# Performance work log

Measured on AMD Instinct MI355X. Metric: run time of the kernel, lower is better.

The kernel has to match this reference:

```python
import jax, jax.numpy as jnp
import numpy as np

B, T, D = 4, 2048, 1024
H, DH = 16, 64

def setup_inputs() -> dict:
    key = jax.random.key(0)
    k1, k2, k3 = jax.random.split(key, 3)
    x = jax.random.normal(k1, (B, T, D), dtype=jnp.float32)
    ln_gamma = jnp.ones((D,), dtype=jnp.float32)
    ln_beta = jnp.zeros((D,), dtype=jnp.float32)
    W_qkv = jax.random.normal(k2, (3 * D, D), dtype=jnp.float32) * (1.0 / np.sqrt(D))
    W_o = jax.random.normal(k3, (D, D), dtype=jnp.float32) * (1.0 / np.sqrt(D))
    return {"x": x, "ln_gamma": ln_gamma, "ln_beta": ln_beta, "W_qkv": W_qkv, "W_o": W_o}

def reference(x, ln_gamma, ln_beta, W_qkv, W_o):
    b, t, d = x.shape
    scale = 1.0 / np.sqrt(DH)
    # pre-LN in fp32 (eps=1e-5, elementwise affine)
    xf = x.astype(jnp.float32)
    mu = jnp.mean(xf, axis=-1, keepdims=True)
    var = jnp.mean(jnp.square(xf - mu), axis=-1, keepdims=True)
    xn = (xf - mu) * jax.lax.rsqrt(var + 1e-5) * ln_gamma + ln_beta
    xn = xn.astype(x.dtype)
    # fused QKV projection (torch Linear: y = x @ W^T), view as (B,T,H,3*DH)
    qkv = jnp.einsum('btd,ed->bte', xn, W_qkv).reshape(b, t, H, 3 * DH)
    Q, K, V = jnp.split(qkv, 3, axis=-1)  # each (B,T,H,DH)
    # scores (B,H,T,T), causal mask, softmax
    scores = jnp.einsum('bqhd,bkhd->bhqk', Q, K) * scale
    causal = jnp.tril(jnp.ones((t, t), dtype=bool))
    scores = jnp.where(causal, scores, -jnp.inf)
    A = jax.nn.softmax(scores, axis=-1)
    ctx = jnp.einsum('bhqk,bkhd->bqhd', A, V).reshape(b, t, d)
    return jnp.einsum('btd,ed->bte', ctx, W_o)
```

## Files before the change

kernel.cpp:

```cpp
#include <hip/hip_runtime.h>


typedef __attribute__((ext_vector_type(8))) short bf8v;
typedef __attribute__((ext_vector_type(4))) float f4v;

#define Tt  2048
#define Dd  1024
#define Hh  16
#define DHh 64

#if __has_builtin(__builtin_amdgcn_exp2f)
#define EXP2(x) __builtin_amdgcn_exp2f(x)
#else
#define EXP2(x) __expf((x) * 0.69314718056f)
#endif

__device__ __forceinline__ ushort f2bf(float f) {
  union { float f; unsigned v; } c; c.f = f;
  unsigned r = c.v + 0x7fffu + ((c.v >> 16) & 1u);
  return (ushort)(r >> 16);
}
__device__ __forceinline__ ushort f2bf_rn(float f) {
  union { float f; unsigned v; } c; c.f = f;
  return (ushort)((c.v + 0x8000u) >> 16);
}
__device__ __forceinline__ f4v zero4() { f4v z; z[0]=z[1]=z[2]=z[3]=0.f; return z; }

__device__ __forceinline__ void gl_lds16(const ushort* g, ushort* l) {
  __builtin_amdgcn_global_load_lds(
      (const __attribute__((address_space(1))) unsigned*)g,
      (__attribute__((address_space(3))) unsigned*)l, 16, 0, 0);
}

__global__ __launch_bounds__(256)
void prep_k(const float* __restrict__ wqkv, ushort* __restrict__ wqkb,
            const float* __restrict__ wo,   ushort* __restrict__ wob,
            const float* __restrict__ x, const float* __restrict__ g,
            const float* __restrict__ bta, ushort* __restrict__ xn) {
  const int bid = blockIdx.x, tid = threadIdx.x;
  if (bid < 4096) {
    const float4* src = (bid < 3072) ? (const float4*)wqkv : (const float4*)wo;
    ushort4* dst      = (bid < 3072) ? (ushort4*)wqkb : (ushort4*)wob;
    const int i = ((bid < 3072) ? bid : (bid - 3072)) * 256 + tid;
    const float4 v = src[i];
    ushort4 o;
    o.x = f2bf(v.x); o.y = f2bf(v.y); o.z = f2bf(v.z); o.w = f2bf(v.w);
    dst[i] = o;
    return;
  }
  const int row = bid - 4096;
  const float4 v = ((const float4*)(x + row * Dd))[tid];
  float s  = v.x + v.y + v.z + v.w;
  float sq = v.x*v.x + v.y*v.y + v.z*v.z + v.w*v.w;
  #pragma unroll
  for (int off = 32; off; off >>= 1) {
    s  += __shfl_down(s,  off, 64);
    sq += __shfl_down(sq, off, 64);
  }
  __shared__ float red[8];
  const int w = tid >> 6, l = tid & 63;
  if (l == 0) { red[w] = s; red[w + 4] = sq; }
  __syncthreads();
  s  = red[0] + red[1] + red[2] + red[3];
  sq = red[4] + red[5] + red[6] + red[7];
  const float mu  = s * (1.0f / Dd);
  const float var = sq * (1.0f / Dd) - mu * mu;
  const float rs  = rsqrtf(var + 1e-5f);
  const float4 gv = ((const float4*)g)[tid];
  const float4 bv = ((const float4*)bta)[tid];
  ushort4 o;
  o.x = f2bf((v.x - mu) * rs * gv.x + bv.x);
  o.y = f2bf((v.y - mu) * rs * gv.y + bv.y);
  o.z = f2bf((v.z - mu) * rs * gv.z + bv.z);
  o.w = f2bf((v.w - mu) * rs * gv.w + bv.w);
  ((ushort4*)(xn + row * Dd))[tid] = o;
}

template<int MODE>
__global__ __launch_bounds__(256)
void gemm128(const ushort* __restrict__ A, const ushort* __restrict__ Bt,
             void* __restrict__ O0v, ushort* __restrict__ O1, ushort* __restrict__ O2,
             int Kd, int nbm) {
  __shared__ ushort As[2][128 * 64], Bs[2][128 * 64];
  const int tid = threadIdx.x;
  const int l = tid & 63, w = tid >> 6, fr = l & 15, fq = l >> 4;
  const int wm = w & 1, wn = w >> 1;
  const int bm = blockIdx.x % nbm, bn = blockIdx.x / nbm;
  const int gr8 = l >> 3, gc8s = ((l & 7) ^ gr8) * 8;
  const int sw = fr & 7;
  const int cA = (fq ^ sw) * 8, cB = ((4 + fq) ^ sw) * 8;
  const int NIT = Kd >> 6;

  f4v acc[4][4];
  #pragma unroll
  for (int m = 0; m < 4; m++)
    #pragma unroll
    for (int n = 0; n < 4; n++) acc[m][n] = zero4();

  auto stage = [&](int it, int bi) {
    const int k0 = it * 64;
    #pragma unroll
    for (int i = 0; i < 4; i++) {
      const int row = w * 32 + i * 8;
      gl_lds16(A  + (bm * 128 + row + gr8) * Kd + k0 + gc8s, &As[bi][row * 64]);
      gl_lds16(Bt + (bn * 128 + row + gr8) * Kd + k0 + gc8s, &Bs[bi][row * 64]);
    }
  };

  stage(0, 0);
  for (int it = 0; it < NIT; ++it) {
    __syncthreads();
    if (it + 1 < NIT) stage(it + 1, (it + 1) & 1);
    const ushort* Ab = As[it & 1];
    const ushort* Bb = Bs[it & 1];
    #pragma unroll
    for (int kk = 0; kk < 2; kk++) {
      const int cs = kk ? cB : cA;
      bf8v af[4], bf[4];
      #pragma unroll
      for (int m = 0; m < 4; m++)
        af[m] = *(const bf8v*)&Ab[(wm * 64 + m * 16 + fr) * 64 + cs];
      #pragma unroll
      for (int n = 0; n < 4; n++)
        bf[n] = *(const bf8v*)&Bb[(wn * 64 + n * 16 + fr) * 64 + cs];
      #pragma unroll
      for (int m = 0; m < 4; m++)
        #pragma unroll
        for (int n = 0; n < 4; n++)
          acc[m][n] = __builtin_amdgcn_mfma_f32_16x16x32_bf16(af[m], bf[n], acc[m][n], 0, 0, 0);
    }
  }

  #pragma unroll
  for (int m = 0; m < 4; m++) {
    const int grow = bm * 128 + wm * 64 + m * 16 + fq * 4;
    #pragma unroll
    for (int n = 0; n < 4; n++) {
      const int e = bn * 128 + wn * 64 + n * 16 + fr;
      #pragma unroll
      for (int r = 0; r < 4; r++) {
        const int row = grow + r;
        if (MODE == 0) {
          const int h = e / 192, inner = e % 192;
          const int sel = inner >> 6, dh = inner & 63;
          if (sel == 2) continue;
          const int bb = row >> 11, t = row & 2047;
          float v = acc[m][n][r];
          if (sel == 0) v *= 0.18033688f;
          ushort* dst = (sel == 0) ? (ushort*)O0v : O1;
          dst[((bb * Hh + h) * Tt + t) * DHh + dh] = f2bf(v);
        } else {
          ((float*)O0v)[row * Dd + e] = acc[m][n][r];
        }
      }
    }
  }

  if (MODE == 0) {
    const int bnm3 = bn % 3;
    if (bnm3 != 0) {
      const int vrun = (bnm3 == 1) ? 0 : 1;
      ushort* Vl = &As[0][0];
      __syncthreads();
      if (wn == vrun) {
        #pragma unroll
        for (int m = 0; m < 4; m++) {
          const int row0 = wm * 64 + m * 16 + fq * 4;
          #pragma unroll
          for (int n = 0; n < 4; n++) {
            const int col = n * 16 + fr;
            ushort4 pk;
            pk.x = f2bf(acc[m][n][0]); pk.y = f2bf(acc[m][n][1]);
            pk.z = f2bf(acc[m][n][2]); pk.w = f2bf(acc[m][n][3]);
            *(ushort4*)&Vl[col * 140 + row0] = pk;
          }
        }
      }
      __syncthreads();
      const int evr = bn * 128 + vrun * 64;
      const int hq  = evr / 192;
      const int bb  = bm >> 4, t0g = (bm & 15) * 128;
      ushort* vdst = O2 + (bb * Hh + hq) * (size_t)(DHh * Tt) + t0g;
      #pragma unroll
      for (int i = 0; i < 4; i++) {
        const int u = i * 256 + tid;
        const int dh = u >> 4, tc = (u & 15) * 8;
        const ushort4 lo = *(const ushort4*)&Vl[dh * 140 + tc];
        const ushort4 hi = *(const ushort4*)&Vl[dh * 140 + tc + 4];
        union { ushort s[8]; uint4 v; } pk;
        pk.s[0] = lo.x; pk.s[1] = lo.y; pk.s[2] = lo.z; pk.s[3] = lo.w;
        pk.s[4] = hi.x; pk.s[5] = hi.y; pk.s[6] = hi.z; pk.s[7] = hi.w;
        *(uint4*)&vdst[dh * Tt + tc] = pk.v;
      }
    }
  }
}

__global__ __launch_bounds__(512)
void attn_k(const ushort* __restrict__ Qb, const ushort* __restrict__ Kb,
            const ushort* __restrict__ Vtg, ushort* __restrict__ ctx) {
  __shared__ ushort QS[128 * 64];
  __shared__ ushort Pb[128 * 68];
  __shared__ ushort Ks[2][64 * 64], Vt[2][64 * 64];
  const int tid = threadIdx.x;
  const int l = tid & 63, w = tid >> 6, fr = l & 15, fq = l >> 4;
  const int bid = blockIdx.x;
  const int hb = (bid & 7) * 8 + (bid >> 6);
  const int u  = (bid >> 3) & 7;
  const int h  = hb & 15, b = hb >> 4;
  const int headbase = hb * Tt * DHh;
  const int gr8 = l >> 3, gc8s = ((l & 7) ^ gr8) * 8;
  const int sw = fr & 7;
  const int cA = (fq ^ sw) * 8, cB = ((4 + fq) ^ sw) * 8;

  auto stageKV = [&](int kt, int bi) {
    const int row = w * 8;
    gl_lds16(Kb  + headbase + (kt * 64 + row + gr8) * DHh + gc8s, &Ks[bi][row * 64]);
    gl_lds16(Vtg + headbase + (row + gr8) * Tt + kt * 64 + gc8s, &Vt[bi][row * 64]);
  };

  for (int half = 0; half < 2; ++half) {
    const int qt = half ? (15 - u) : u;
    const int qrow0w = qt * 128 + w * 16;

    if (half) __syncthreads();

    #pragma unroll
    for (int i = 0; i < 2; i++) {
      const int row = w * 16 + i * 8;
      gl_lds16(Qb + headbase + (qt * 128 + row + gr8) * DHh + gc8s, &QS[row * 64]);
    }
    stageKV(0, 0);
    __syncthreads();

    bf8v aq[2];
    aq[0] = *(const bf8v*)&QS[(w * 16 + fr) * 64 + cA];
    aq[1] = *(const bf8v*)&QS[(w * 16 + fr) * 64 + cB];
    __asm__ __volatile__("" ::: "memory");

    f4v o[4];
    #pragma unroll
    for (int n = 0; n < 4; n++) o[n] = zero4();
    float lsum = 0.f;

    const int ktmax = 2 * qt + 1;
    for (int kt = 0; kt <= ktmax; ++kt) {
      if (kt) __syncthreads();
      if (kt < ktmax) stageKV(kt + 1, (kt + 1) & 1);
      const ushort* K_ = Ks[kt & 1];
      const ushort* V_ = Vt[kt & 1];

      if (kt * 64 <= qrow0w + 15) {
        f4v scT[4];
        #pragma unroll
        for (int n = 0; n < 4; n++) scT[n] = zero4();
        __builtin_amdgcn_s_setprio(1);
        #pragma unroll
        for (int nt = 0; nt < 4; nt++) {
          const bf8v k0 = *(const bf8v*)&K_[(nt * 16 + fr) * 64 + cA];
          const bf8v k1 = *(const bf8v*)&K_[(nt * 16 + fr) * 64 + cB];
          scT[nt] = __builtin_amdgcn_mfma_f32_16x16x32_bf16(k0, aq[0], scT[nt], 0, 0, 0);
          scT[nt] = __builtin_amdgcn_mfma_f32_16x16x32_bf16(k1, aq[1], scT[nt], 0, 0, 0);
        }
        __builtin_amdgcn_s_setprio(0);

        if (kt * 64 + 63 > qrow0w) {
          const int q0 = qrow0w + fr;
          #pragma unroll
          for (int nt = 0; nt < 4; nt++) {
            const int kc0 = kt * 64 + nt * 16 + fq * 4;
            #pragma unroll
            for (int r = 0; r < 4; r++)
              if (kc0 + r > q0) scT[nt][r] = -1e30f;
          }
        }

        {
          const int prow = w * 16 + fr;
          ushort* pbase = &Pb[prow * 68 + fq * 4];
          #pragma unroll
          for (int nt = 0; nt < 4; nt++) {
            const float p0 = EXP2(scT[nt][0]), p1 = EXP2(scT[nt][1]);
            const float p2 = EXP2(scT[nt][2]), p3 = EXP2(scT[nt][3]);
            ushort4 pk;
            pk.x = f2bf_rn(p0); pk.y = f2bf_rn(p1);
            pk.z = f2bf_rn(p2); pk.w = f2bf_rn(p3);
            *(ushort4*)(pbase + nt * 16) = pk;
            lsum += (p0 + p1) + (p2 + p3);
          }
        }

        __asm__ __volatile__("" ::: "memory");

        __builtin_amdgcn_s_setprio(1);
        #pragma unroll
        for (int s = 0; s < 2; s++) {
          const bf8v ap = *(const bf8v*)&Pb[(w * 16 + fr) * 68 + s * 32 + fq * 8];
          #pragma unroll
          for (int nt = 0; nt < 4; nt++) {
            const bf8v bv2 = *(const bf8v*)&V_[(nt * 16 + fr) * 64 + (s ? cB : cA)];
            o[nt] = __builtin_amdgcn_mfma_f32_16x16x32_bf16(ap, bv2, o[nt], 0, 0, 0);
          }
        }
        __builtin_amdgcn_s_setprio(0);
      }
    }

    float t = lsum;
    t += __shfl_xor(t, 16, 64);
    t += __shfl_xor(t, 32, 64);
    const float inv = 1.0f / t;
    #pragma unroll
    for (int r = 0; r < 4; r++) {
      const float iv = __shfl(inv, 20 * fq + r, 64);
      const int rowg = b * Tt + qt * 128 + w * 16 + fq * 4 + r;
      #pragma unroll
      for (int nt = 0; nt < 4; nt++)
        ctx[rowg * Dd + h * DHh + nt * 16 + fr] = f2bf(o[nt][r] * iv);
    }
  }
}

extern "C" void kernel_launch(void* const* d_in, const int* in_sizes, int n_in,
                              void* d_out, int out_size, void* d_ws, size_t ws_size,
                              hipStream_t stream) {
  const float* x    = (const float*)d_in[0];
  const float* g    = (const float*)d_in[1];
  const float* bta  = (const float*)d_in[2];
  const float* wqkv = (const float*)d_in[3];
  const float* wo   = (const float*)d_in[4];

  const int NROW = 4 * Tt;
  const int NQ   = 4 * Hh * Tt * DHh;
  ushort* xn   = (ushort*)d_ws;
  ushort* Qb   = xn + NROW * Dd;
  ushort* Kb   = Qb + NQ;
  ushort* Vb   = Kb + NQ;
  ushort* ctx  = Vb + NQ;
  ushort* wqkb = ctx + NROW * Dd;
  ushort* wob  = wqkb + 3 * Dd * Dd;

  prep_k<<<3072 + 1024 + NROW, 256, 0, stream>>>(wqkv, wqkb, wo, wob, x, g, bta, xn);
  gemm128<0><<<64 * 24, 256, 0, stream>>>(xn, wqkb, Qb, Kb, Vb, Dd, 64);
  attn_k<<<4 * Hh * (Tt / 128) / 2, 512, 0, stream>>>(Qb, Kb, Vb, ctx);
  gemm128<1><<<64 * 8, 256, 0, stream>>>(ctx, wob, (void*)d_out, nullptr, nullptr, Dd, 64);
}
```

Measured before the change: 231.3 us.

## Widen GEMM block tile to 128x256 and restructure V-transpose epilogue

Both projection GEMMs now compute 128x256 output tiles per block instead of 128x128, so each wave holds a 4x8 grid of MFMA accumulators. This halves the grid size and doubles the reuse of each staged A tile, which should cut global and LDS traffic per output. The fused QKV epilogue is reworked to find up to two 64-column V chunks per tile and transpose each through a separate LDS region. The trade-off is more LDS (about 96KB) and more accumulator registers per block, so one block per CU, and fewer blocks to spread across the CUs.

```diff
diff --git a/kernel.cpp b/kernel.cpp
--- a/kernel.cpp
+++ b/kernel.cpp
@@ -77,11 +77,12 @@
 }
 
 template<int MODE>
-__global__ __launch_bounds__(256)
-void gemm128(const ushort* __restrict__ A, const ushort* __restrict__ Bt,
-             void* __restrict__ O0v, ushort* __restrict__ O1, ushort* __restrict__ O2,
-             int Kd, int nbm) {
-  __shared__ ushort As[2][128 * 64], Bs[2][128 * 64];
+__global__ __launch_bounds__(256, 1)
+void gemmB(const ushort* __restrict__ A, const ushort* __restrict__ Bt,
+           void* __restrict__ O0v, ushort* __restrict__ O1, ushort* __restrict__ O2,
+           int Kd, int nbm) {
+  __shared__ ushort As[2][128 * 64];
+  __shared__ ushort Bs[2][256 * 64];
   const int tid = threadIdx.x;
   const int l = tid & 63, w = tid >> 6, fr = l & 15, fq = l >> 4;
   const int wm = w & 1, wn = w >> 1;
@@ -91,19 +92,23 @@
   const int cA = (fq ^ sw) * 8, cB = ((4 + fq) ^ sw) * 8;
   const int NIT = Kd >> 6;
 
-  f4v acc[4][4];
+  f4v acc[4][8];
   #pragma unroll
   for (int m = 0; m < 4; m++)
     #pragma unroll
-    for (int n = 0; n < 4; n++) acc[m][n] = zero4();
+    for (int n = 0; n < 8; n++) acc[m][n] = zero4();
 
   auto stage = [&](int it, int bi) {
     const int k0 = it * 64;
     #pragma unroll
     for (int i = 0; i < 4; i++) {
       const int row = w * 32 + i * 8;
-      gl_lds16(A  + (bm * 128 + row + gr8) * Kd + k0 + gc8s, &As[bi][row * 64]);
-      gl_lds16(Bt + (bn * 128 + row + gr8) * Kd + k0 + gc8s, &Bs[bi][row * 64]);
+      gl_lds16(A + (bm * 128 + row + gr8) * Kd + k0 + gc8s, &As[bi][row * 64]);
+    }
+    #pragma unroll
+    for (int i = 0; i < 8; i++) {
+      const int row = w * 64 + i * 8;
+      gl_lds16(Bt + (bn * 256 + row + gr8) * Kd + k0 + gc8s, &Bs[bi][row * 64]);
     }
   };
 
@@ -116,17 +121,17 @@
     #pragma unroll
     for (int kk = 0; kk < 2; kk++) {
       const int cs = kk ? cB : cA;
-      bf8v af[4], bf[4];
+      bf8v af[4], bf[8];
       #pragma unroll
       for (int m = 0; m < 4; m++)
         af[m] = *(const bf8v*)&Ab[(wm * 64 + m * 16 + fr) * 64 + cs];
       #pragma unroll
-      for (int n = 0; n < 4; n++)
-        bf[n] = *(const bf8v*)&Bb[(wn * 64 + n * 16 + fr) * 64 + cs];
+      for (int n = 0; n < 8; n++)
+        bf[n] = *(const bf8v*)&Bb[(wn * 128 + n * 16 + fr) * 64 + cs];
       #pragma unroll
       for (int m = 0; m < 4; m++)
         #pragma unroll
-        for (int n = 0; n < 4; n++)
+        for (int n = 0; n < 8; n++)
           acc[m][n] = __builtin_amdgcn_mfma_f32_16x16x32_bf16(af[m], bf[n], acc[m][n], 0, 0, 0);
     }
   }
@@ -135,8 +140,8 @@
   for (int m = 0; m < 4; m++) {
     const int grow = bm * 128 + wm * 64 + m * 16 + fq * 4;
     #pragma unroll
-    for (int n = 0; n < 4; n++) {
-      const int e = bn * 128 + wn * 64 + n * 16 + fr;
+    for (int n = 0; n < 8; n++) {
+      const int e = bn * 256 + wn * 128 + n * 16 + fr;
       #pragma unroll
       for (int r = 0; r < 4; r++) {
         const int row = grow + r;
@@ -157,33 +162,40 @@
   }
 
   if (MODE == 0) {
-    const int bnm3 = bn % 3;
-    if (bnm3 != 0) {
-      const int vrun = (bnm3 == 1) ? 0 : 1;
-      ushort* Vl = &As[0][0];
-      __syncthreads();
-      if (wn == vrun) {
+    int vqs[2]; int nv = 0;
+    #pragma unroll
+    for (int q = 0; q < 4; q++)
+      if (((bn * 4 + q) % 3) == 2) vqs[nv++] = q;
+    __syncthreads();
+    for (int i = 0; i < nv; i++) {
+      const int q = vqs[i];
+      ushort* Vl = (i == 0) ? &As[0][0] : &Bs[0][0];
+      if (wn == (q >> 1)) {
         #pragma unroll
         for (int m = 0; m < 4; m++) {
           const int row0 = wm * 64 + m * 16 + fq * 4;
           #pragma unroll
-          for (int n = 0; n < 4; n++) {
-            const int col = n * 16 + fr;
+          for (int j = 0; j < 4; j++) {
+            const int n = (q & 1) * 4 + j;
+            const int dh = j * 16 + fr;
             ushort4 pk;
             pk.x = f2bf(acc[m][n][0]); pk.y = f2bf(acc[m][n][1]);
             pk.z = f2bf(acc[m][n][2]); pk.w = f2bf(acc[m][n][3]);
-            *(ushort4*)&Vl[col * 140 + row0] = pk;
+            *(ushort4*)&Vl[dh * 140 + row0] = pk;
           }
         }
       }
-      __syncthreads();
-      const int evr = bn * 128 + vrun * 64;
-      const int hq  = evr / 192;
-      const int bb  = bm >> 4, t0g = (bm & 15) * 128;
-      ushort* vdst = O2 + (bb * Hh + hq) * (size_t)(DHh * Tt) + t0g;
-      #pragma unroll
-      for (int i = 0; i < 4; i++) {
-        const int u = i * 256 + tid;
+    }
+    __syncthreads();
+    for (int i = 0; i < nv; i++) {
+      const int q = vqs[i];
+      const ushort* Vl = (i == 0) ? &As[0][0] : &Bs[0][0];
+      const int h  = (bn * 256 + q * 64) / 192;
+      const int bb = bm >> 4, t0g = (bm & 15) * 128;
+      ushort* vdst = O2 + (bb * Hh + h) * (size_t)(DHh * Tt) + t0g;
+      #pragma unroll
+      for (int u4 = 0; u4 < 4; u4++) {
+        const int u = u4 * 256 + tid;
         const int dh = u >> 4, tc = (u & 15) * 8;
         const ushort4 lo = *(const ushort4*)&Vl[dh * 140 + tc];
         const ushort4 hi = *(const ushort4*)&Vl[dh * 140 + tc + 4];
@@ -341,7 +353,7 @@
   ushort* wob  = wqkb + 3 * Dd * Dd;
 
   prep_k<<<3072 + 1024 + NROW, 256, 0, stream>>>(wqkv, wqkb, wo, wob, x, g, bta, xn);
-  gemm128<0><<<64 * 24, 256, 0, stream>>>(xn, wqkb, Qb, Kb, Vb, Dd, 64);
+  gemmB<0><<<64 * 12, 256, 0, stream>>>(xn, wqkb, Qb, Kb, Vb, Dd, 64);
   attn_k<<<4 * Hh * (Tt / 128) / 2, 512, 0, stream>>>(Qb, Kb, Vb, ctx);
-  gemm128<1><<<64 * 8, 256, 0, stream>>>(ctx, wob, (void*)d_out, nullptr, nullptr, Dd, 64);
-}
+  gemmB<1><<<64 * 4, 256, 0, stream>>>(ctx, wob, (void*)d_out, nullptr, nullptr, Dd, 64);
+}
```

Result: slower. 458.3 us (+98.2%).
